# Performance work log

Hardware: AMD Instinct MI355X
Metric: run time of the kernel (lower is better)

Reference implementation:

```python
import jax, jax.numpy as jnp
import numpy as np

B_SZ, L_SEQ, D_MODEL, D_STATE = 4, 2048, 1024, 16


def setup_inputs() -> dict:
    key = jax.random.key(0)
    ks = jax.random.split(key, 6)
    x = jax.random.normal(ks[0], (B_SZ, L_SEQ, D_MODEL), jnp.float32)
    # HiPPO-inspired init: A_log = log(arange(1..n)).clamp(min=-7), broadcast over channels
    A_log = jnp.clip(jnp.log(jnp.arange(1, D_STATE + 1, dtype=jnp.float32)), -7.0, None)
    A_log = jnp.broadcast_to(A_log[None, :], (D_MODEL, D_STATE)).astype(jnp.float32)
    B_param = 0.02 * jax.random.normal(ks[1], (D_MODEL, D_STATE), jnp.float32)
    C_param = 0.02 * jax.random.normal(ks[2], (D_MODEL, D_STATE), jnp.float32)
    log_dt = 0.01 * jax.random.normal(ks[3], (D_MODEL,), jnp.float32) - 4.0
    in_w = jax.random.normal(ks[4], (2 * D_MODEL, D_MODEL), jnp.float32) / np.sqrt(D_MODEL).astype(np.float32)
    in_b = jnp.zeros((2 * D_MODEL,), jnp.float32)
    out_w = jax.random.normal(ks[5], (D_MODEL, D_MODEL), jnp.float32) / np.sqrt(D_MODEL).astype(np.float32)
    out_b = jnp.zeros((D_MODEL,), jnp.float32)
    ln_g = jnp.ones((D_MODEL,), jnp.float32)
    ln_b = jnp.zeros((D_MODEL,), jnp.float32)
    return {"x": x, "A_log": A_log, "B_param": B_param, "C_param": C_param,
            "log_dt": log_dt, "in_w": in_w, "in_b": in_b, "out_w": out_w,
            "out_b": out_b, "ln_g": ln_g, "ln_b": ln_b}


def _ssm_scan(u, A_log, B_param, C_param, log_dt):
    # u: (B, L, D). Builds kernel h[t,d] = sum_n A_bar[d,n]^t * C[d,n]*B[d,n]*dt[d]
    # and applies a causal depthwise convolution (via FFT; same math as conv1d).
    L = u.shape[1]
    dt = jnp.clip(jnp.exp(log_dt), 1e-4, 1.0)                      # (D,)
    A_bar = jnp.exp(-jnp.exp(A_log) * dt[:, None])                 # ZOH discretisation (D,N)
    A_bar = jnp.clip(A_bar, 1e-8, 1.0 - 1e-8)
    log_A = jnp.log(A_bar)                                         # (D,N)
    t_idx = jnp.arange(L, dtype=jnp.float32)                       # (L,)
    A_powers = jnp.exp(t_idx[:, None, None] * log_A[None, :, :])   # (L,D,N)
    cb_dt = C_param * B_param * dt[:, None]                        # (D,N)
    kernel = jnp.einsum('ldn,dn->ld', A_powers, cb_dt)             # (L,D)
    # causal conv: y[b,t,d] = sum_{tau<=t} kernel[tau,d] * u[b,t-tau,d]
    n_fft = 2 * L
    Kf = jnp.fft.rfft(kernel, n=n_fft, axis=0)                     # (n_fft/2+1, D)
    Uf = jnp.fft.rfft(u, n=n_fft, axis=1)                          # (B, n_fft/2+1, D)
    y = jnp.fft.irfft(Uf * Kf[None], n=n_fft, axis=1)[:, :L]       # (B,L,D)
    return y.astype(u.dtype)


def reference(x, A_log, B_param, C_param, log_dt, in_w, in_b, out_w, out_b, ln_g, ln_b):
    x = x.astype(jnp.float32)
    residual = x
    # LayerNorm (eps=1e-5)
    mu = jnp.mean(x, axis=-1, keepdims=True)
    var = jnp.mean(jnp.square(x - mu), axis=-1, keepdims=True)
    xn = (x - mu) * jax.lax.rsqrt(var + 1e-5) * ln_g + ln_b
    xz = xn @ in_w.T + in_b                                        # (B,L,2D)
    x_proj, z = xz[..., :D_MODEL], xz[..., D_MODEL:]
    z = jax.nn.silu(z)
    y = _ssm_scan(x_proj, A_log, B_param, C_param, log_dt)
    y = y * z
    y = y @ out_w.T + out_b
    # dropout is identity in eval mode
    return jnp.clip(y + residual, -10.0, 10.0)
```

## Files before the change

kernel.cpp:

```cpp
#include <hip/hip_runtime.h>
#include <hip/hip_bf16.h>

#define D_MODEL 1024
#define D_STATE 16
#define L_SEQ 2048
#define B_SZ 4
#define M_ROWS (B_SZ * L_SEQ)
#define N_CHUNK 32
#define C_LEN 64

typedef __attribute__((ext_vector_type(8))) short short8;
typedef __attribute__((ext_vector_type(4))) float f32x4;
typedef unsigned int u32;
#define GLOBAL_AS __attribute__((address_space(1)))
#define LDS_AS __attribute__((address_space(3)))

static __device__ __forceinline__ unsigned short f2bf(float f) {
    unsigned int u = __float_as_uint(f);
    unsigned int r = (u + 0x7FFFu + ((u >> 16) & 1u)) >> 16;
    return (unsigned short)r;
}
static __device__ __forceinline__ float bf2f(unsigned short u) {
    return __uint_as_float(((unsigned int)u) << 16);
}

__global__ void conv_bf16_kernel(const float* __restrict__ src,
                                 unsigned short* __restrict__ dst, int n4) {
    int i = blockIdx.x * blockDim.x + threadIdx.x;
    if (i < n4) {
        float4 v = ((const float4*)src)[i];
        ushort4 o;
        o.x = f2bf(v.x); o.y = f2bf(v.y); o.z = f2bf(v.z); o.w = f2bf(v.w);
        ((ushort4*)dst)[i] = o;
    }
}

__global__ __launch_bounds__(256) void ln_kernel(const float* __restrict__ x,
                                                 const float* __restrict__ g,
                                                 const float* __restrict__ b,
                                                 unsigned short* __restrict__ xn) {
    int row = blockIdx.x;
    int t = threadIdx.x;
    const float4* xr = (const float4*)(x + (size_t)row * D_MODEL);
    float4 v = xr[t];
    float s  = v.x + v.y + v.z + v.w;
    float ss = v.x * v.x + v.y * v.y + v.z * v.z + v.w * v.w;
    #pragma unroll
    for (int o = 32; o > 0; o >>= 1) {
        s  += __shfl_down(s,  o);
        ss += __shfl_down(ss, o);
    }
    __shared__ float sbuf[8];
    int wid = t >> 6;
    if ((t & 63) == 0) { sbuf[wid] = s; sbuf[4 + wid] = ss; }
    __syncthreads();
    float S  = sbuf[0] + sbuf[1] + sbuf[2] + sbuf[3];
    float SS = sbuf[4] + sbuf[5] + sbuf[6] + sbuf[7];
    float mu  = S * (1.0f / D_MODEL);
    float var = SS * (1.0f / D_MODEL) - mu * mu;
    float inv = rsqrtf(var + 1e-5f);
    float4 gv = ((const float4*)g)[t];
    float4 bv = ((const float4*)b)[t];
    ushort4 o;
    o.x = f2bf((v.x - mu) * inv * gv.x + bv.x);
    o.y = f2bf((v.y - mu) * inv * gv.y + bv.y);
    o.z = f2bf((v.z - mu) * inv * gv.z + bv.z);
    o.w = f2bf((v.w - mu) * inv * gv.w + bv.w);
    ((ushort4*)(xn + (size_t)row * D_MODEL))[t] = o;
}

__global__ __launch_bounds__(256, 2) void gemm1_kernel(const unsigned short* __restrict__ A,
                                                       const unsigned short* __restrict__ Bt,
                                                       const float* __restrict__ bias,
                                                       unsigned short* __restrict__ u_bf,
                                                       unsigned short* __restrict__ zs) {
    __shared__ unsigned short lA[128 * 32];
    __shared__ unsigned short lB[256 * 32];
    const int K = D_MODEL;

    int t = threadIdx.x;
    int lane = t & 63;
    int wave = t >> 6;
    int wm = wave >> 1, wn = wave & 1;
    int m0 = blockIdx.y * 128;
    int n0 = blockIdx.x * 256;
    int row = lane & 15;
    int quad = lane >> 4;

    int sr = t >> 2;
    int sc = ((t & 3) ^ ((t >> 3) & 3)) * 8;
    const unsigned short* gA0 = A + (size_t)(m0 + sr) * K + sc;
    const unsigned short* gA1 = A + (size_t)(m0 + 64 + sr) * K + sc;
    const unsigned short* gB0 = Bt + (size_t)(n0 + sr) * K + sc;
    const unsigned short* gB1 = Bt + (size_t)(n0 + 64 + sr) * K + sc;
    const unsigned short* gB2 = Bt + (size_t)(n0 + 128 + sr) * K + sc;
    const unsigned short* gB3 = Bt + (size_t)(n0 + 192 + sr) * K + sc;

    int offA[4], offB[8];
    #pragma unroll
    for (int i = 0; i < 4; i++) {
        int r6 = i * 16 + row;
        int slot = r6 * 4 + (quad ^ ((r6 >> 1) & 3));
        offA[i] = wm * 2048 + slot * 8;
    }
    #pragma unroll
    for (int j = 0; j < 8; j++) {
        int r8 = wn * 128 + j * 16 + row;
        int half = r8 >> 6, r6 = r8 & 63;
        int slot = r6 * 4 + (quad ^ ((r6 >> 1) & 3));
        offB[j] = half * 2048 + slot * 8;
    }

    f32x4 acc[4][8] = {};

    for (int kk = 0; kk < K; kk += 32) {
        __builtin_amdgcn_global_load_lds((const GLOBAL_AS u32*)(gA0 + kk),
                                         (LDS_AS u32*)&lA[t * 8], 16, 0, 0);
        __builtin_amdgcn_global_load_lds((const GLOBAL_AS u32*)(gA1 + kk),
                                         (LDS_AS u32*)&lA[2048 + t * 8], 16, 0, 0);
        __builtin_amdgcn_global_load_lds((const GLOBAL_AS u32*)(gB0 + kk),
                                         (LDS_AS u32*)&lB[t * 8], 16, 0, 0);
        __builtin_amdgcn_global_load_lds((const GLOBAL_AS u32*)(gB1 + kk),
                                         (LDS_AS u32*)&lB[2048 + t * 8], 16, 0, 0);
        __builtin_amdgcn_global_load_lds((const GLOBAL_AS u32*)(gB2 + kk),
                                         (LDS_AS u32*)&lB[4096 + t * 8], 16, 0, 0);
        __builtin_amdgcn_global_load_lds((const GLOBAL_AS u32*)(gB3 + kk),
                                         (LDS_AS u32*)&lB[6144 + t * 8], 16, 0, 0);
        __syncthreads();

        short8 a[4];
        #pragma unroll
        for (int i = 0; i < 4; i++) a[i] = *(const short8*)&lA[offA[i]];
        #pragma unroll
        for (int j = 0; j < 8; j++) {
            short8 b = *(const short8*)&lB[offB[j]];
            #pragma unroll
            for (int i = 0; i < 4; i++)
                acc[i][j] = __builtin_amdgcn_mfma_f32_16x16x32_bf16(a[i], b, acc[i][j], 0, 0, 0);
        }
        __syncthreads();
    }

    int col = row;
    #pragma unroll
    for (int j = 0; j < 8; j++) {
        int n = n0 + wn * 128 + j * 16 + col;
        float bs = bias[n];
        #pragma unroll
        for (int i = 0; i < 4; i++) {
            #pragma unroll
            for (int r = 0; r < 4; r++) {
                int m = m0 + wm * 64 + i * 16 + quad * 4 + r;
                float v = acc[i][j][r] + bs;
                if (n < D_MODEL) {
                    u_bf[(size_t)m * D_MODEL + n] = f2bf(v);
                } else {
                    float sv = v / (1.0f + __expf(-v));
                    zs[(size_t)m * D_MODEL + (n - D_MODEL)] = f2bf(sv);
                }
            }
        }
    }
}

__global__ __launch_bounds__(256) void gemm2_kernel(const unsigned short* __restrict__ A,
                                                    const unsigned short* __restrict__ Bt,
                                                    const float* __restrict__ bias,
                                                    float* __restrict__ out_f,
                                                    const float* __restrict__ resid) {
    __shared__ unsigned short lA[128 * 32];
    __shared__ unsigned short lB[128 * 32];
    const int K = D_MODEL;

    int t = threadIdx.x;
    int lane = t & 63;
    int wave = t >> 6;
    int wm = wave >> 1, wn = wave & 1;
    int m0 = blockIdx.y * 128;
    int n0 = blockIdx.x * 128;
    int row = lane & 15;
    int quad = lane >> 4;

    int sr = t >> 2;
    int sc = ((t & 3) ^ ((t >> 3) & 3)) * 8;
    const unsigned short* gA0 = A + (size_t)(m0 + sr) * K + sc;
    const unsigned short* gA1 = A + (size_t)(m0 + 64 + sr) * K + sc;
    const unsigned short* gB0 = Bt + (size_t)(n0 + sr) * K + sc;
    const unsigned short* gB1 = Bt + (size_t)(n0 + 64 + sr) * K + sc;

    int offA[4], offB[4];
    #pragma unroll
    for (int i = 0; i < 4; i++) {
        int r6 = i * 16 + row;
        int slot = r6 * 4 + (quad ^ ((r6 >> 1) & 3));
        offA[i] = wm * 2048 + slot * 8;
        offB[i] = wn * 2048 + slot * 8;
    }

    f32x4 acc[4][4] = {};

    for (int kk = 0; kk < K; kk += 32) {
        __builtin_amdgcn_global_load_lds((const GLOBAL_AS u32*)(gA0 + kk),
                                         (LDS_AS u32*)&lA[t * 8], 16, 0, 0);
        __builtin_amdgcn_global_load_lds((const GLOBAL_AS u32*)(gA1 + kk),
                                         (LDS_AS u32*)&lA[2048 + t * 8], 16, 0, 0);
        __builtin_amdgcn_global_load_lds((const GLOBAL_AS u32*)(gB0 + kk),
                                         (LDS_AS u32*)&lB[t * 8], 16, 0, 0);
        __builtin_amdgcn_global_load_lds((const GLOBAL_AS u32*)(gB1 + kk),
                                         (LDS_AS u32*)&lB[2048 + t * 8], 16, 0, 0);
        __syncthreads();

        short8 a[4], b[4];
        #pragma unroll
        for (int i = 0; i < 4; i++) a[i] = *(const short8*)&lA[offA[i]];
        #pragma unroll
        for (int j = 0; j < 4; j++) b[j] = *(const short8*)&lB[offB[j]];
        #pragma unroll
        for (int i = 0; i < 4; i++)
            #pragma unroll
            for (int j = 0; j < 4; j++)
                acc[i][j] = __builtin_amdgcn_mfma_f32_16x16x32_bf16(a[i], b[j], acc[i][j], 0, 0, 0);
        __syncthreads();
    }

    int col = row;
    #pragma unroll
    for (int i = 0; i < 4; i++) {
        #pragma unroll
        for (int j = 0; j < 4; j++) {
            int n = n0 + wn * 64 + j * 16 + col;
            float bs = bias[n];
            #pragma unroll
            for (int r = 0; r < 4; r++) {
                int m = m0 + wm * 64 + i * 16 + quad * 4 + r;
                float y = acc[i][j][r] + bs + resid[(size_t)m * D_MODEL + n];
                y = fminf(10.0f, fmaxf(-10.0f, y));
                out_f[(size_t)m * D_MODEL + n] = y;
            }
        }
    }
}

static __device__ __forceinline__ void load_params(const float* __restrict__ A_log,
                                                   const float* __restrict__ log_dt,
                                                   int d, float* ab, float& dt_out) {
    float dt = fminf(1.0f, fmaxf(1e-4f, __expf(log_dt[d])));
    #pragma unroll
    for (int n = 0; n < D_STATE; n++) {
        float a = __expf(-__expf(A_log[d * D_STATE + n]) * dt);
        ab[n] = fminf(1.0f - 1e-8f, fmaxf(1e-8f, a));
    }
    dt_out = dt;
}

__global__ __launch_bounds__(256) void scan1_kernel(const unsigned short* __restrict__ u,
                                                    const float* __restrict__ A_log,
                                                    const float* __restrict__ log_dt,
                                                    float* __restrict__ s_local) {
    int gid = blockIdx.x * 256 + threadIdx.x;
    int d = gid & (D_MODEL - 1);
    int c = (gid >> 10) & (N_CHUNK - 1);
    int b = gid >> 15;

    float ab[D_STATE], dt;
    load_params(A_log, log_dt, d, ab, dt);

    float s[D_STATE];
    #pragma unroll
    for (int n = 0; n < D_STATE; n++) s[n] = 0.0f;

    const unsigned short* up = u + ((size_t)(b * L_SEQ + c * C_LEN)) * D_MODEL + d;
    for (int t = 0; t < C_LEN; t++) {
        float uv = bf2f(up[(size_t)t * D_MODEL]);
        #pragma unroll
        for (int n = 0; n < D_STATE; n++) s[n] = fmaf(ab[n], s[n], uv);
    }
    float* sl = s_local + ((size_t)(b * N_CHUNK + c) * D_STATE) * D_MODEL + d;
    #pragma unroll
    for (int n = 0; n < D_STATE; n++) sl[(size_t)n * D_MODEL] = s[n];
}

__global__ __launch_bounds__(256) void scan_combine_kernel(const float* __restrict__ s_local,
                                                           const float* __restrict__ A_log,
                                                           const float* __restrict__ log_dt,
                                                           float* __restrict__ s_init) {
    int gid = blockIdx.x * 256 + threadIdx.x;
    int d = gid & (D_MODEL - 1);
    int n = (gid >> 10) & (D_STATE - 1);
    int b = gid >> 14;

    float dt = fminf(1.0f, fmaxf(1e-4f, __expf(log_dt[d])));
    float a = __expf(-__expf(A_log[d * D_STATE + n]) * dt);
    a = fminf(1.0f - 1e-8f, fmaxf(1e-8f, a));
    float aP = a;
    #pragma unroll
    for (int q = 0; q < 6; q++) aP = aP * aP;

    float s = 0.0f;
    size_t stride_c = (size_t)D_STATE * D_MODEL;
    const float* sl = s_local + ((size_t)b * N_CHUNK * D_STATE + n) * D_MODEL + d;
    float* si = s_init + ((size_t)b * N_CHUNK * D_STATE + n) * D_MODEL + d;
    si[0] = 0.0f;
    for (int c = 1; c < N_CHUNK; c++) {
        s = fmaf(aP, s, sl[(size_t)(c - 1) * stride_c]);
        si[(size_t)c * stride_c] = s;
    }
}

__global__ __launch_bounds__(256) void scan2_kernel(const unsigned short* __restrict__ u,
                                                    const unsigned short* __restrict__ zs,
                                                    const float* __restrict__ A_log,
                                                    const float* __restrict__ Bp,
                                                    const float* __restrict__ Cp,
                                                    const float* __restrict__ log_dt,
                                                    const float* __restrict__ s_init,
                                                    unsigned short* __restrict__ yz) {
    int gid = blockIdx.x * 256 + threadIdx.x;
    int d = gid & (D_MODEL - 1);
    int c = (gid >> 10) & (N_CHUNK - 1);
    int b = gid >> 15;

    float ab[D_STATE], dt;
    load_params(A_log, log_dt, d, ab, dt);
    float cb[D_STATE];
    #pragma unroll
    for (int n = 0; n < D_STATE; n++)
        cb[n] = Cp[d * D_STATE + n] * Bp[d * D_STATE + n] * dt;

    float s[D_STATE];
    const float* si = s_init + ((size_t)(b * N_CHUNK + c) * D_STATE) * D_MODEL + d;
    #pragma unroll
    for (int n = 0; n < D_STATE; n++) s[n] = si[(size_t)n * D_MODEL];

    size_t m0 = (size_t)(b * L_SEQ + c * C_LEN);
    const unsigned short* up = u + m0 * D_MODEL + d;
    const unsigned short* zp = zs + m0 * D_MODEL + d;
    unsigned short* yp = yz + m0 * D_MODEL + d;

    for (int t = 0; t < C_LEN; t++) {
        float uv = bf2f(up[(size_t)t * D_MODEL]);
        #pragma unroll
        for (int n = 0; n < D_STATE; n++) s[n] = fmaf(ab[n], s[n], uv);
        float y = 0.0f;
        #pragma unroll
        for (int n = 0; n < D_STATE; n++) y = fmaf(cb[n], s[n], y);
        float zv = bf2f(zp[(size_t)t * D_MODEL]);
        yp[(size_t)t * D_MODEL] = f2bf(y * zv);
    }
}

extern "C" void kernel_launch(void* const* d_in, const int* in_sizes, int n_in,
                              void* d_out, int out_size, void* d_ws, size_t ws_size,
                              hipStream_t stream) {
    const float* x       = (const float*)d_in[0];
    const float* A_log   = (const float*)d_in[1];
    const float* B_param = (const float*)d_in[2];
    const float* C_param = (const float*)d_in[3];
    const float* log_dt  = (const float*)d_in[4];
    const float* in_w    = (const float*)d_in[5];
    const float* in_b    = (const float*)d_in[6];
    const float* out_w   = (const float*)d_in[7];
    const float* out_b   = (const float*)d_in[8];
    const float* ln_g    = (const float*)d_in[9];
    const float* ln_b    = (const float*)d_in[10];
    float* out = (float*)d_out;

    char* ws = (char*)d_ws;
    size_t off = 0;
    unsigned short* xn = (unsigned short*)(ws + off); off += (size_t)M_ROWS * D_MODEL * 2;
    unsigned short* w1 = (unsigned short*)(ws + off); off += (size_t)2 * D_MODEL * D_MODEL * 2;
    unsigned short* u  = (unsigned short*)(ws + off); off += (size_t)M_ROWS * D_MODEL * 2;
    unsigned short* zs = (unsigned short*)(ws + off); off += (size_t)M_ROWS * D_MODEL * 2;
    unsigned short* yz = (unsigned short*)(ws + off); off += (size_t)M_ROWS * D_MODEL * 2;
    unsigned short* w2 = (unsigned short*)(ws + off); off += (size_t)D_MODEL * D_MODEL * 2;
    float* s_local = (float*)(ws + off); off += (size_t)B_SZ * N_CHUNK * D_STATE * D_MODEL * 4;
    float* s_init  = (float*)(ws + off); off += (size_t)B_SZ * N_CHUNK * D_STATE * D_MODEL * 4;

    {
        int n4 = 2 * D_MODEL * D_MODEL / 4;
        conv_bf16_kernel<<<(n4 + 255) / 256, 256, 0, stream>>>(in_w, w1, n4);
    }
    {
        int n4 = D_MODEL * D_MODEL / 4;
        conv_bf16_kernel<<<(n4 + 255) / 256, 256, 0, stream>>>(out_w, w2, n4);
    }

    ln_kernel<<<M_ROWS, 256, 0, stream>>>(x, ln_g, ln_b, xn);

    gemm1_kernel<<<dim3(2 * D_MODEL / 256, M_ROWS / 128), 256, 0, stream>>>(
        xn, w1, in_b, u, zs);

    scan1_kernel<<<(B_SZ * N_CHUNK * D_MODEL) / 256, 256, 0, stream>>>(u, A_log, log_dt, s_local);
    scan_combine_kernel<<<(B_SZ * D_STATE * D_MODEL) / 256, 256, 0, stream>>>(s_local, A_log, log_dt, s_init);
    scan2_kernel<<<(B_SZ * N_CHUNK * D_MODEL) / 256, 256, 0, stream>>>(
        u, zs, A_log, B_param, C_param, log_dt, s_init, yz);

    gemm2_kernel<<<dim3(D_MODEL / 128, M_ROWS / 128), 256, 0, stream>>>(
        yz, w2, out_b, out, x);
}
```

Measured before the change: 223.0 us.

## Double-buffer GEMM LDS tiles with register prefetch instead of direct global-to-LDS loads

Both GEMM kernels stop using global_load_lds. They now prefetch the next K-slice into registers while the current slice is consumed from one of two LDS buffers, which removes the second barrier per iteration. The goal is to overlap global memory latency with MFMA work. In exchange it costs more registers (24 extra VGPRs in gemm1, which has launch_bounds 256,2), doubles LDS use, and adds explicit ds_write instructions.

```diff
diff --git a/kernel.cpp b/kernel.cpp
--- a/kernel.cpp
+++ b/kernel.cpp
@@ -12,8 +12,7 @@
 typedef __attribute__((ext_vector_type(8))) short short8;
 typedef __attribute__((ext_vector_type(4))) float f32x4;
 typedef unsigned int u32;
-#define GLOBAL_AS __attribute__((address_space(1)))
-#define LDS_AS __attribute__((address_space(3)))
+typedef __attribute__((ext_vector_type(4))) u32 u32x4;
 
 static __device__ __forceinline__ unsigned short f2bf(float f) {
     unsigned int u = __float_as_uint(f);
@@ -74,8 +73,8 @@
                                                        const float* __restrict__ bias,
                                                        unsigned short* __restrict__ u_bf,
                                                        unsigned short* __restrict__ zs) {
-    __shared__ unsigned short lA[128 * 32];
-    __shared__ unsigned short lB[256 * 32];
+    __shared__ unsigned short lA[2][128 * 32];
+    __shared__ unsigned short lB[2][256 * 32];
     const int K = D_MODEL;
 
     int t = threadIdx.x;
@@ -111,34 +110,45 @@
         offB[j] = half * 2048 + slot * 8;
     }
 
+    u32x4 pa0 = *(const u32x4*)gA0;
+    u32x4 pa1 = *(const u32x4*)gA1;
+    u32x4 pb0 = *(const u32x4*)gB0;
+    u32x4 pb1 = *(const u32x4*)gB1;
+    u32x4 pb2 = *(const u32x4*)gB2;
+    u32x4 pb3 = *(const u32x4*)gB3;
+
     f32x4 acc[4][8] = {};
 
     for (int kk = 0; kk < K; kk += 32) {
-        __builtin_amdgcn_global_load_lds((const GLOBAL_AS u32*)(gA0 + kk),
-                                         (LDS_AS u32*)&lA[t * 8], 16, 0, 0);
-        __builtin_amdgcn_global_load_lds((const GLOBAL_AS u32*)(gA1 + kk),
-                                         (LDS_AS u32*)&lA[2048 + t * 8], 16, 0, 0);
-        __builtin_amdgcn_global_load_lds((const GLOBAL_AS u32*)(gB0 + kk),
-                                         (LDS_AS u32*)&lB[t * 8], 16, 0, 0);
-        __builtin_amdgcn_global_load_lds((const GLOBAL_AS u32*)(gB1 + kk),
-                                         (LDS_AS u32*)&lB[2048 + t * 8], 16, 0, 0);
-        __builtin_amdgcn_global_load_lds((const GLOBAL_AS u32*)(gB2 + kk),
-                                         (LDS_AS u32*)&lB[4096 + t * 8], 16, 0, 0);
-        __builtin_amdgcn_global_load_lds((const GLOBAL_AS u32*)(gB3 + kk),
-                                         (LDS_AS u32*)&lB[6144 + t * 8], 16, 0, 0);
+        int buf = (kk >> 5) & 1;
+        unsigned short* sA = lA[buf];
+        unsigned short* sB = lB[buf];
+        *(u32x4*)&sA[t * 8]        = pa0;
+        *(u32x4*)&sA[2048 + t * 8] = pa1;
+        *(u32x4*)&sB[t * 8]        = pb0;
+        *(u32x4*)&sB[2048 + t * 8] = pb1;
+        *(u32x4*)&sB[4096 + t * 8] = pb2;
+        *(u32x4*)&sB[6144 + t * 8] = pb3;
         __syncthreads();
-
+        int kn = kk + 32;
+        if (kn < K) {
+            pa0 = *(const u32x4*)(gA0 + kn);
+            pa1 = *(const u32x4*)(gA1 + kn);
+            pb0 = *(const u32x4*)(gB0 + kn);
+            pb1 = *(const u32x4*)(gB1 + kn);
+            pb2 = *(const u32x4*)(gB2 + kn);
+            pb3 = *(const u32x4*)(gB3 + kn);
+        }
         short8 a[4];
         #pragma unroll
-        for (int i = 0; i < 4; i++) a[i] = *(const short8*)&lA[offA[i]];
+        for (int i = 0; i < 4; i++) a[i] = *(const short8*)&sA[offA[i]];
         #pragma unroll
         for (int j = 0; j < 8; j++) {
-            short8 b = *(const short8*)&lB[offB[j]];
+            short8 b = *(const short8*)&sB[offB[j]];
             #pragma unroll
             for (int i = 0; i < 4; i++)
                 acc[i][j] = __builtin_amdgcn_mfma_f32_16x16x32_bf16(a[i], b, acc[i][j], 0, 0, 0);
         }
-        __syncthreads();
     }
 
     int col = row;
@@ -168,8 +178,8 @@
                                                     const float* __restrict__ bias,
                                                     float* __restrict__ out_f,
                                                     const float* __restrict__ resid) {
-    __shared__ unsigned short lA[128 * 32];
-    __shared__ unsigned short lB[128 * 32];
+    __shared__ unsigned short lA[2][128 * 32];
+    __shared__ unsigned short lB[2][128 * 32];
     const int K = D_MODEL;
 
     int t = threadIdx.x;
@@ -197,30 +207,39 @@
         offB[i] = wn * 2048 + slot * 8;
     }
 
+    u32x4 pa0 = *(const u32x4*)gA0;
+    u32x4 pa1 = *(const u32x4*)gA1;
+    u32x4 pb0 = *(const u32x4*)gB0;
+    u32x4 pb1 = *(const u32x4*)gB1;
+
     f32x4 acc[4][4] = {};
 
     for (int kk = 0; kk < K; kk += 32) {
-        __builtin_amdgcn_global_load_lds((const GLOBAL_AS u32*)(gA0 + kk),
-                                         (LDS_AS u32*)&lA[t * 8], 16, 0, 0);
-        __builtin_amdgcn_global_load_lds((const GLOBAL_AS u32*)(gA1 + kk),
-                                         (LDS_AS u32*)&lA[2048 + t * 8], 16, 0, 0);
-        __builtin_amdgcn_global_load_lds((const GLOBAL_AS u32*)(gB0 + kk),
-                                         (LDS_AS u32*)&lB[t * 8], 16, 0, 0);
-        __builtin_amdgcn_global_load_lds((const GLOBAL_AS u32*)(gB1 + kk),
-                                         (LDS_AS u32*)&lB[2048 + t * 8], 16, 0, 0);
+        int buf = (kk >> 5) & 1;
+        unsigned short* sA = lA[buf];
+        unsigned short* sB = lB[buf];
+        *(u32x4*)&sA[t * 8]        = pa0;
+        *(u32x4*)&sA[2048 + t * 8] = pa1;
+        *(u32x4*)&sB[t * 8]        = pb0;
+        *(u32x4*)&sB[2048 + t * 8] = pb1;
         __syncthreads();
-
+        int kn = kk + 32;
+        if (kn < K) {
+            pa0 = *(const u32x4*)(gA0 + kn);
+            pa1 = *(const u32x4*)(gA1 + kn);
+            pb0 = *(const u32x4*)(gB0 + kn);
+            pb1 = *(const u32x4*)(gB1 + kn);
+        }
         short8 a[4], b[4];
         #pragma unroll
-        for (int i = 0; i < 4; i++) a[i] = *(const short8*)&lA[offA[i]];
-        #pragma unroll
-        for (int j = 0; j < 4; j++) b[j] = *(const short8*)&lB[offB[j]];
+        for (int i = 0; i < 4; i++) a[i] = *(const short8*)&sA[offA[i]];
+        #pragma unroll
+        for (int j = 0; j < 4; j++) b[j] = *(const short8*)&sB[offB[j]];
         #pragma unroll
         for (int i = 0; i < 4; i++)
             #pragma unroll
             for (int j = 0; j < 4; j++)
                 acc[i][j] = __builtin_amdgcn_mfma_f32_16x16x32_bf16(a[i], b[j], acc[i][j], 0, 0, 0);
-        __syncthreads();
     }
 
     int col = row;
```

After: 222.1 us. About the same (-0.4%).

## Double-buffer GEMM LDS tiles with register prefetch and swap grid order

Applied to the files above, without the earlier changes.

Both GEMM kernels drop the direct global-to-LDS loads. They now prefetch the next K-slices into registers, store them into two alternating LDS buffers, and need one barrier per step instead of two. This aims to hide global-load latency behind the MFMA work. The grid axes are also swapped so consecutive blocks walk along M rather than N, which changes L2 reuse of the weight tiles. The cost is higher register pressure from 12 (gemm1) or 8 (gemm2) prefetched u32x4 registers and double the LDS footprint, which could lower occupancy for gemm1 under launch_bounds(256,2).

```diff
diff --git a/kernel.cpp b/kernel.cpp
--- a/kernel.cpp
+++ b/kernel.cpp
@@ -12,8 +12,9 @@
 typedef __attribute__((ext_vector_type(8))) short short8;
 typedef __attribute__((ext_vector_type(4))) float f32x4;
 typedef unsigned int u32;
-#define GLOBAL_AS __attribute__((address_space(1)))
-#define LDS_AS __attribute__((address_space(3)))
+typedef __attribute__((ext_vector_type(4))) u32 u32x4;
+
+#define BAR() asm volatile("s_waitcnt lgkmcnt(0)\n\ts_barrier" ::: "memory")
 
 static __device__ __forceinline__ unsigned short f2bf(float f) {
     unsigned int u = __float_as_uint(f);
@@ -74,16 +75,16 @@
                                                        const float* __restrict__ bias,
                                                        unsigned short* __restrict__ u_bf,
                                                        unsigned short* __restrict__ zs) {
-    __shared__ unsigned short lA[128 * 32];
-    __shared__ unsigned short lB[256 * 32];
+    __shared__ unsigned short lA[2][128 * 32];
+    __shared__ unsigned short lB[2][256 * 32];
     const int K = D_MODEL;
 
     int t = threadIdx.x;
     int lane = t & 63;
     int wave = t >> 6;
     int wm = wave >> 1, wn = wave & 1;
-    int m0 = blockIdx.y * 128;
-    int n0 = blockIdx.x * 256;
+    int m0 = blockIdx.x * 128;
+    int n0 = blockIdx.y * 256;
     int row = lane & 15;
     int quad = lane >> 4;
 
@@ -113,32 +114,65 @@
 
     f32x4 acc[4][8] = {};
 
-    for (int kk = 0; kk < K; kk += 32) {
-        __builtin_amdgcn_global_load_lds((const GLOBAL_AS u32*)(gA0 + kk),
-                                         (LDS_AS u32*)&lA[t * 8], 16, 0, 0);
-        __builtin_amdgcn_global_load_lds((const GLOBAL_AS u32*)(gA1 + kk),
-                                         (LDS_AS u32*)&lA[2048 + t * 8], 16, 0, 0);
-        __builtin_amdgcn_global_load_lds((const GLOBAL_AS u32*)(gB0 + kk),
-                                         (LDS_AS u32*)&lB[t * 8], 16, 0, 0);
-        __builtin_amdgcn_global_load_lds((const GLOBAL_AS u32*)(gB1 + kk),
-                                         (LDS_AS u32*)&lB[2048 + t * 8], 16, 0, 0);
-        __builtin_amdgcn_global_load_lds((const GLOBAL_AS u32*)(gB2 + kk),
-                                         (LDS_AS u32*)&lB[4096 + t * 8], 16, 0, 0);
-        __builtin_amdgcn_global_load_lds((const GLOBAL_AS u32*)(gB3 + kk),
-                                         (LDS_AS u32*)&lB[6144 + t * 8], 16, 0, 0);
-        __syncthreads();
-
-        short8 a[4];
-        #pragma unroll
-        for (int i = 0; i < 4; i++) a[i] = *(const short8*)&lA[offA[i]];
-        #pragma unroll
-        for (int j = 0; j < 8; j++) {
-            short8 b = *(const short8*)&lB[offB[j]];
-            #pragma unroll
-            for (int i = 0; i < 4; i++)
-                acc[i][j] = __builtin_amdgcn_mfma_f32_16x16x32_bf16(a[i], b, acc[i][j], 0, 0, 0);
-        }
-        __syncthreads();
+    u32x4 PA[6], PB[6];
+    PA[0] = *(const u32x4*)gA0;        PA[1] = *(const u32x4*)gA1;
+    PA[2] = *(const u32x4*)gB0;        PA[3] = *(const u32x4*)gB1;
+    PA[4] = *(const u32x4*)gB2;        PA[5] = *(const u32x4*)gB3;
+    PB[0] = *(const u32x4*)(gA0 + 32); PB[1] = *(const u32x4*)(gA1 + 32);
+    PB[2] = *(const u32x4*)(gB0 + 32); PB[3] = *(const u32x4*)(gB1 + 32);
+    PB[4] = *(const u32x4*)(gB2 + 32); PB[5] = *(const u32x4*)(gB3 + 32);
+
+    for (int kk = 0; kk < K; kk += 64) {
+        *(u32x4*)&lA[0][t * 8]        = PA[0];
+        *(u32x4*)&lA[0][2048 + t * 8] = PA[1];
+        *(u32x4*)&lB[0][t * 8]        = PA[2];
+        *(u32x4*)&lB[0][2048 + t * 8] = PA[3];
+        *(u32x4*)&lB[0][4096 + t * 8] = PA[4];
+        *(u32x4*)&lB[0][6144 + t * 8] = PA[5];
+        if (kk + 64 < K) {
+            int kn = kk + 64;
+            PA[0] = *(const u32x4*)(gA0 + kn); PA[1] = *(const u32x4*)(gA1 + kn);
+            PA[2] = *(const u32x4*)(gB0 + kn); PA[3] = *(const u32x4*)(gB1 + kn);
+            PA[4] = *(const u32x4*)(gB2 + kn); PA[5] = *(const u32x4*)(gB3 + kn);
+        }
+        BAR();
+        {
+            short8 a[4];
+            #pragma unroll
+            for (int i = 0; i < 4; i++) a[i] = *(const short8*)&lA[0][offA[i]];
+            #pragma unroll
+            for (int j = 0; j < 8; j++) {
+                short8 b = *(const short8*)&lB[0][offB[j]];
+                #pragma unroll
+                for (int i = 0; i < 4; i++)
+                    acc[i][j] = __builtin_amdgcn_mfma_f32_16x16x32_bf16(a[i], b, acc[i][j], 0, 0, 0);
+            }
+        }
+        *(u32x4*)&lA[1][t * 8]        = PB[0];
+        *(u32x4*)&lA[1][2048 + t * 8] = PB[1];
+        *(u32x4*)&lB[1][t * 8]        = PB[2];
+        *(u32x4*)&lB[1][2048 + t * 8] = PB[3];
+        *(u32x4*)&lB[1][4096 + t * 8] = PB[4];
+        *(u32x4*)&lB[1][6144 + t * 8] = PB[5];
+        if (kk + 96 < K) {
+            int kn = kk + 96;
+            PB[0] = *(const u32x4*)(gA0 + kn); PB[1] = *(const u32x4*)(gA1 + kn);
+            PB[2] = *(const u32x4*)(gB0 + kn); PB[3] = *(const u32x4*)(gB1 + kn);
+            PB[4] = *(const u32x4*)(gB2 + kn); PB[5] = *(const u32x4*)(gB3 + kn);
+        }
+        BAR();
+        {
+            short8 a[4];
+            #pragma unroll
+            for (int i = 0; i < 4; i++) a[i] = *(const short8*)&lA[1][offA[i]];
+            #pragma unroll
+            for (int j = 0; j < 8; j++) {
+                short8 b = *(const short8*)&lB[1][offB[j]];
+                #pragma unroll
+                for (int i = 0; i < 4; i++)
+                    acc[i][j] = __builtin_amdgcn_mfma_f32_16x16x32_bf16(a[i], b, acc[i][j], 0, 0, 0);
+            }
+        }
     }
 
     int col = row;
@@ -168,16 +202,16 @@
                                                     const float* __restrict__ bias,
                                                     float* __restrict__ out_f,
                                                     const float* __restrict__ resid) {
-    __shared__ unsigned short lA[128 * 32];
-    __shared__ unsigned short lB[128 * 32];
+    __shared__ unsigned short lA[2][128 * 32];
+    __shared__ unsigned short lB[2][128 * 32];
     const int K = D_MODEL;
 
     int t = threadIdx.x;
     int lane = t & 63;
     int wave = t >> 6;
     int wm = wave >> 1, wn = wave & 1;
-    int m0 = blockIdx.y * 128;
-    int n0 = blockIdx.x * 128;
+    int m0 = blockIdx.x * 128;
+    int n0 = blockIdx.y * 128;
     int row = lane & 15;
     int quad = lane >> 4;
 
@@ -199,28 +233,57 @@
 
     f32x4 acc[4][4] = {};
 
-    for (int kk = 0; kk < K; kk += 32) {
-        __builtin_amdgcn_global_load_lds((const GLOBAL_AS u32*)(gA0 + kk),
-                                         (LDS_AS u32*)&lA[t * 8], 16, 0, 0);
-        __builtin_amdgcn_global_load_lds((const GLOBAL_AS u32*)(gA1 + kk),
-                                         (LDS_AS u32*)&lA[2048 + t * 8], 16, 0, 0);
-        __builtin_amdgcn_global_load_lds((const GLOBAL_AS u32*)(gB0 + kk),
-                                         (LDS_AS u32*)&lB[t * 8], 16, 0, 0);
-        __builtin_amdgcn_global_load_lds((const GLOBAL_AS u32*)(gB1 + kk),
-                                         (LDS_AS u32*)&lB[2048 + t * 8], 16, 0, 0);
-        __syncthreads();
-
-        short8 a[4], b[4];
-        #pragma unroll
-        for (int i = 0; i < 4; i++) a[i] = *(const short8*)&lA[offA[i]];
-        #pragma unroll
-        for (int j = 0; j < 4; j++) b[j] = *(const short8*)&lB[offB[j]];
-        #pragma unroll
-        for (int i = 0; i < 4; i++)
-            #pragma unroll
-            for (int j = 0; j < 4; j++)
-                acc[i][j] = __builtin_amdgcn_mfma_f32_16x16x32_bf16(a[i], b[j], acc[i][j], 0, 0, 0);
-        __syncthreads();
+    u32x4 PA[4], PB[4];
+    PA[0] = *(const u32x4*)gA0;        PA[1] = *(const u32x4*)gA1;
+    PA[2] = *(const u32x4*)gB0;        PA[3] = *(const u32x4*)gB1;
+    PB[0] = *(const u32x4*)(gA0 + 32); PB[1] = *(const u32x4*)(gA1 + 32);
+    PB[2] = *(const u32x4*)(gB0 + 32); PB[3] = *(const u32x4*)(gB1 + 32);
+
+    for (int kk = 0; kk < K; kk += 64) {
+        *(u32x4*)&lA[0][t * 8]        = PA[0];
+        *(u32x4*)&lA[0][2048 + t * 8] = PA[1];
+        *(u32x4*)&lB[0][t * 8]        = PA[2];
+        *(u32x4*)&lB[0][2048 + t * 8] = PA[3];
+        if (kk + 64 < K) {
+            int kn = kk + 64;
+            PA[0] = *(const u32x4*)(gA0 + kn); PA[1] = *(const u32x4*)(gA1 + kn);
+            PA[2] = *(const u32x4*)(gB0 + kn); PA[3] = *(const u32x4*)(gB1 + kn);
+        }
+        BAR();
+        {
+            short8 a[4], b[4];
+            #pragma unroll
+            for (int i = 0; i < 4; i++) a[i] = *(const short8*)&lA[0][offA[i]];
+            #pragma unroll
+            for (int j = 0; j < 4; j++) b[j] = *(const short8*)&lB[0][offB[j]];
+            #pragma unroll
+            for (int i = 0; i < 4; i++)
+                #pragma unroll
+                for (int j = 0; j < 4; j++)
+                    acc[i][j] = __builtin_amdgcn_mfma_f32_16x16x32_bf16(a[i], b[j], acc[i][j], 0, 0, 0);
+        }
+        *(u32x4*)&lA[1][t * 8]        = PB[0];
+        *(u32x4*)&lA[1][2048 + t * 8] = PB[1];
+        *(u32x4*)&lB[1][t * 8]        = PB[2];
+        *(u32x4*)&lB[1][2048 + t * 8] = PB[3];
+        if (kk + 96 < K) {
+            int kn = kk + 96;
+            PB[0] = *(const u32x4*)(gA0 + kn); PB[1] = *(const u32x4*)(gA1 + kn);
+            PB[2] = *(const u32x4*)(gB0 + kn); PB[3] = *(const u32x4*)(gB1 + kn);
+        }
+        BAR();
+        {
+            short8 a[4], b[4];
+            #pragma unroll
+            for (int i = 0; i < 4; i++) a[i] = *(const short8*)&lA[1][offA[i]];
+            #pragma unroll
+            for (int j = 0; j < 4; j++) b[j] = *(const short8*)&lB[1][offB[j]];
+            #pragma unroll
+            for (int i = 0; i < 4; i++)
+                #pragma unroll
+                for (int j = 0; j < 4; j++)
+                    acc[i][j] = __builtin_amdgcn_mfma_f32_16x16x32_bf16(a[i], b[j], acc[i][j], 0, 0, 0);
+        }
     }
 
     int col = row;
@@ -387,7 +450,7 @@
 
     ln_kernel<<<M_ROWS, 256, 0, stream>>>(x, ln_g, ln_b, xn);
 
-    gemm1_kernel<<<dim3(2 * D_MODEL / 256, M_ROWS / 128), 256, 0, stream>>>(
+    gemm1_kernel<<<dim3(M_ROWS / 128, 2 * D_MODEL / 256), 256, 0, stream>>>(
         xn, w1, in_b, u, zs);
 
     scan1_kernel<<<(B_SZ * N_CHUNK * D_MODEL) / 256, 256, 0, stream>>>(u, A_log, log_dt, s_local);
@@ -395,6 +458,6 @@
     scan2_kernel<<<(B_SZ * N_CHUNK * D_MODEL) / 256, 256, 0, stream>>>(
         u, zs, A_log, B_param, C_param, log_dt, s_init, yz);
 
-    gemm2_kernel<<<dim3(D_MODEL / 128, M_ROWS / 128), 256, 0, stream>>>(
+    gemm2_kernel<<<dim3(M_ROWS / 128, D_MODEL / 128), 256, 0, stream>>>(
         yz, w2, out_b, out, x);
 }
```

After: 215.9 us. -3.2%, faster.
